# Optimization experiments

Measured on AMD Instinct MI355X. Metric: run time of the kernel, lower is better.

## Reference

```python
import jax, jax.numpy as jnp
import numpy as np

# --- module constants (from init_kwargs) ---
BETA = 0.95
UTE = 1.0001
DELAY = 7
CHOSEN_W1 = 0.5
THRESHOLD = 1.0      # snntorch Leaky default threshold
ALPHA = 2.0          # snntorch ATan surrogate default alpha
T, B = 4096, 4096
SPIKE_PROB = 0.02    # sparse binary spike trains


@jax.custom_vjp
def spike_fn(x):
    # Heaviside forward; ATan surrogate gradient in backward (snntorch default)
    return (x > 0).astype(x.dtype)

def _spike_fwd(x):
    return spike_fn(x), x

def _spike_bwd(x, g):
    return (g * (ALPHA / 2.0) / (1.0 + (jnp.pi / 2.0 * ALPHA * x) ** 2),)

spike_fn.defvjp(_spike_fwd, _spike_bwd)


def setup_inputs() -> dict:
    key = jax.random.key(0)
    k1, _ = jax.random.split(key)
    spike_seq = (jax.random.uniform(k1, (T, B, 2)) < SPIKE_PROB).astype(jnp.float32)
    # calculate_weights(delay): w1 = chosen_w1; w2 = ute - beta**delay * w1
    w1 = CHOSEN_W1
    w2 = UTE - BETA ** DELAY * w1
    W = jnp.array([[w1, w2]], dtype=jnp.float32)  # fc.weight, shape [1, 2]
    return {"spike_seq": spike_seq, "W": W}


def reference(spike_seq, W):
    # spike_seq: [T, B, 2], W: [1, 2] -> spk_rec: [T, B, 1]
    # Precompute all linear currents in one GEMM (same math as per-step fc)
    cur_seq = jnp.einsum('tbi,oi->tbo', spike_seq, W)  # [T, B, 1]

    def step(mem, cur):
        # snntorch Leaky (reset_mechanism='subtract'):
        #   reset computed from PREVIOUS mem (detached heaviside)
        reset = (mem > THRESHOLD).astype(mem.dtype)
        mem_new = BETA * mem + cur - reset * THRESHOLD
        spk = spike_fn(mem_new - THRESHOLD)
        return mem_new, spk

    mem0 = jnp.zeros((spike_seq.shape[1], 1), dtype=spike_seq.dtype)
    _, spk_rec = jax.lax.scan(step, mem0, cur_seq)
    return spk_rec
```

## Files before the change

kernel.cpp:

```cpp
#include <hip/hip_runtime.h>
#include <stdint.h>


#define T_STEPS 4096
#define B_NEUR  4096
#define NCHUNK  32
#define CH_W    8
#define WARM_W  48
#define KG      (T_STEPS / 16)

typedef float f4v __attribute__((ext_vector_type(4)));

__global__ __launch_bounds__(256) void fmfm_compress(
    const f4v*  __restrict__ sp4,
    uint32_t*   __restrict__ codes)
{
    const int tid = blockIdx.x * 256 + threadIdx.x;
    const int b2  = tid & (B_NEUR / 2 - 1);
    const int kg  = tid >> 11;
    const f4v* p = sp4 + (size_t)kg * 16 * (B_NEUR / 2) + b2;
    uint32_t we = 0, wo = 0;
    #pragma unroll
    for (int i = 0; i < 16; ++i) {
        f4v s = __builtin_nontemporal_load(p + (size_t)i * (B_NEUR / 2));
        uint32_t ce = (s.x != 0.0f ? 1u : 0u) | (s.y != 0.0f ? 2u : 0u);
        uint32_t co = (s.z != 0.0f ? 1u : 0u) | (s.w != 0.0f ? 2u : 0u);
        we |= ce << (2 * i);
        wo |= co << (2 * i);
    }
    *reinterpret_cast<uint2*>(codes + (size_t)kg * B_NEUR + 2 * b2) =
        make_uint2(we, wo);
}

__global__ __launch_bounds__(256) void fmfm_scanA(
    const uint32_t* __restrict__ codes,
    const float*    __restrict__ W,
    float*          __restrict__ out,
    uint4*          __restrict__ spec)
{
    __shared__ float2 lut2[16];

    const float w1  = W[0];
    const float w2  = W[1];
    const float w12 = __fadd_rn(w1, w2);

    if (threadIdx.x < 16) {
        uint32_t e = threadIdx.x;
        uint32_t c0 = e & 3u, c1 = (e >> 2) & 3u;
        float2 v;
        v.x = (c0 & 1u) ? ((c0 & 2u) ? w12 : w1) : ((c0 & 2u) ? w2 : 0.0f);
        v.y = (c1 & 1u) ? ((c1 & 2u) ? w12 : w1) : ((c1 & 2u) ? w2 : 0.0f);
        lut2[e] = v;
    }
    __syncthreads();

    const int tid = blockIdx.x * 256 + threadIdx.x;
    const int b   = tid & (B_NEUR - 1);
    const int c   = tid >> 12;
    const int body_w0 = c * CH_W;
    const int w_start = (body_w0 >= WARM_W) ? body_w0 - WARM_W : 0;
    const int w_end   = body_w0 + CH_W;
    const uint32_t* cp = codes + b;

#define CLD(IDX) cp[(size_t)((IDX) < w_end ? (IDX) : (w_end - 1)) * B_NEUR]
#define DECODE2(WORD, D)                                                  \
    {                                                                     \
        _Pragma("unroll")                                                 \
        for (int _j = 0; _j < 8; ++_j)                                    \
            D[_j] = lut2[((WORD) >> (4 * _j)) & 0xFu];                    \
    }
#define STEPN(CUR)                                                        \
    {                                                                     \
        float _m = __fsub_rn(__fadd_rn(__fmul_rn(0.95f, mem), (CUR)),     \
                             rst);                                        \
        rst = (_m > 1.0f) ? 1.0f : 0.0f;                                  \
        mem = _m;                                                         \
    }
#define STEPS_(CUR, Q, K)                                                 \
    {                                                                     \
        float _m = __fsub_rn(__fadd_rn(__fmul_rn(0.95f, mem), (CUR)),     \
                             rst);                                        \
        rst = (_m > 1.0f) ? 1.0f : 0.0f;                                  \
        mem = _m;                                                         \
        __builtin_nontemporal_store(rst, (Q) + (size_t)(K) * B_NEUR);     \
    }
#define CHAIN16N(D)                                                       \
    {                                                                     \
        _Pragma("unroll")                                                 \
        for (int _j = 0; _j < 8; ++_j) { STEPN(D[_j].x) STEPN(D[_j].y) }  \
    }
#define CHAIN16S(D, WIDX)                                                 \
    {                                                                     \
        float* _q = out + (size_t)(WIDX) * 16 * B_NEUR + b;               \
        _Pragma("unroll")                                                 \
        for (int _j = 0; _j < 8; ++_j) {                                  \
            STEPS_(D[_j].x, _q, 2 * _j)                                   \
            STEPS_(D[_j].y, _q, 2 * _j + 1)                               \
        }                                                                 \
    }

    uint32_t pa = CLD(w_start);
    uint32_t pb = CLD(w_start + 1);
    uint32_t pc = CLD(w_start + 2);
    uint32_t pd = CLD(w_start + 3);

    float2 dA[8], dB[8];
    DECODE2(pa, dA)

    float mem = 0.0f, rst = 0.0f;

    for (int iw = w_start; iw < body_w0; iw += 2) {
        uint32_t t0 = CLD(iw + 4);
        DECODE2(pb, dB)
        CHAIN16N(dA)
        pa = pb; pb = pc; pc = pd; pd = t0;
        uint32_t t1 = CLD(iw + 5);
        DECODE2(pb, dA)
        CHAIN16N(dB)
        pa = pb; pb = pc; pc = pd; pd = t1;
    }

    const float sm = mem;
    const float sr = rst;

    for (int iw = body_w0; iw < w_end; iw += 2) {
        uint32_t t0 = CLD(iw + 4);
        DECODE2(pb, dB)
        CHAIN16S(dA, iw)
        pa = pb; pb = pc; pc = pd; pd = t0;
        uint32_t t1 = CLD(iw + 5);
        DECODE2(pb, dA)
        CHAIN16S(dB, iw + 1)
        pa = pb; pb = pc; pc = pd; pd = t1;
    }

    uint4 sv;
    sv.x = __float_as_uint(sm);
    sv.y = (sr != 0.0f) ? 1u : 0u;
    sv.z = __float_as_uint(mem);
    sv.w = (rst != 0.0f) ? 1u : 0u;
    spec[(size_t)c * B_NEUR + b] = sv;

#undef CLD
#undef DECODE2
#undef STEPN
#undef STEPS_
#undef CHAIN16N
#undef CHAIN16S
}

__global__ __launch_bounds__(64) void fmfm_scanB(
    const uint32_t* __restrict__ codes,
    const float*    __restrict__ W,
    float*          __restrict__ out,
    const uint4*    __restrict__ spec)
{
    const int b = blockIdx.x * 64 + threadIdx.x;
    const float w1  = W[0];
    const float w2  = W[1];
    const float w12 = __fadd_rn(w1, w2);

    float mem = 0.0f, rst = 0.0f;
    uint4 sn = spec[b];
    for (int c = 0; c < NCHUNK; ++c) {
        uint4 s = sn;
        if (c + 1 < NCHUNK) sn = spec[(size_t)(c + 1) * B_NEUR + b];
        bool ok = (s.x == __float_as_uint(mem)) &&
                  ((s.y != 0u) == (rst != 0.0f));
        if (ok) {
            mem = __uint_as_float(s.z);
            rst = s.w ? 1.0f : 0.0f;
        } else {
            for (int wi = 0; wi < CH_W; ++wi) {
                uint32_t w = codes[(size_t)(c * CH_W + wi) * B_NEUR + b];
                float* q = out + (size_t)(c * CH_W + wi) * 16 * B_NEUR + b;
                #pragma unroll
                for (int j = 0; j < 16; ++j) {
                    uint32_t cc = (w >> (2 * j)) & 3u;
                    float cur = (cc & 1u) ? ((cc & 2u) ? w12 : w1)
                                          : ((cc & 2u) ? w2 : 0.0f);
                    float m = __fsub_rn(__fadd_rn(__fmul_rn(0.95f, mem), cur),
                                        rst);
                    rst = (m > 1.0f) ? 1.0f : 0.0f;
                    mem = m;
                    q[(size_t)j * B_NEUR] = rst;
                }
            }
        }
    }
}

__global__ __launch_bounds__(64) void fmfm_scan_fused(
    const float2* __restrict__ sp, const float* __restrict__ W,
    float* __restrict__ out)
{
    const int b = blockIdx.x * 64 + threadIdx.x;
    const float w1 = W[0];
    const float w2 = W[1];
    const float2* p = sp + b;
    float* q = out + b;
    float mem = 0.0f, rst = 0.0f;
    #pragma unroll 8
    for (int t = 0; t < T_STEPS; ++t) {
        float2 s = p[(size_t)t * B_NEUR];
        float cur = __fadd_rn(__fmul_rn(s.x, w1), __fmul_rn(s.y, w2));
        float m = __fsub_rn(__fadd_rn(__fmul_rn(0.95f, mem), cur), rst);
        float spk = (m > 1.0f) ? 1.0f : 0.0f;
        q[(size_t)t * B_NEUR] = spk;
        mem = m;
        rst = spk;
    }
}

extern "C" void kernel_launch(void* const* d_in, const int* in_sizes, int n_in,
                              void* d_out, int out_size, void* d_ws, size_t ws_size,
                              hipStream_t stream) {
    const f4v*   sp4 = (const f4v*)d_in[0];
    const float* W   = (const float*)d_in[1];
    float*       out = (float*)d_out;

    const size_t codes_bytes = (size_t)KG * B_NEUR * 4;
    const size_t spec_bytes  = (size_t)NCHUNK * B_NEUR * 16;
    if (ws_size < codes_bytes + spec_bytes) {
        fmfm_scan_fused<<<dim3(B_NEUR / 64), dim3(64), 0, stream>>>(
            (const float2*)d_in[0], W, out);
        return;
    }
    uint32_t* codes = (uint32_t*)d_ws;
    uint4*    spec  = (uint4*)((char*)d_ws + codes_bytes);

    fmfm_compress<<<dim3(KG * (B_NEUR / 2) / 256), dim3(256), 0, stream>>>(sp4, codes);
    fmfm_scanA<<<dim3(NCHUNK * B_NEUR / 256), dim3(256), 0, stream>>>(codes, W, out, spec);
    fmfm_scanB<<<dim3(B_NEUR / 64), dim3(64), 0, stream>>>(codes, W, out, spec);
}
```

Before: 60.21 us.

## Pack spike bits in LDS and write output as coalesced float4 stores

Result: faster. 58.04 us (-3.6%).

```diff
diff --git a/kernel.cpp b/kernel.cpp
--- a/kernel.cpp
+++ b/kernel.cpp
@@ -4,8 +4,8 @@
 
 #define T_STEPS 4096
 #define B_NEUR  4096
-#define NCHUNK  32
-#define CH_W    8
+#define NCHUNK  16
+#define CH_W    16
 #define WARM_W  48
 #define KG      (T_STEPS / 16)
 
@@ -38,7 +38,8 @@
     float*          __restrict__ out,
     uint4*          __restrict__ spec)
 {
-    __shared__ float2 lut2[16];
+    __shared__ float2   lut2[16];
+    __shared__ uint32_t lbits[256];
 
     const float w1  = W[0];
     const float w2  = W[1];
@@ -57,6 +58,7 @@
     const int tid = blockIdx.x * 256 + threadIdx.x;
     const int b   = tid & (B_NEUR - 1);
     const int c   = tid >> 12;
+    const int b0  = (blockIdx.x * 256) & (B_NEUR - 1);
     const int body_w0 = c * CH_W;
     const int w_start = (body_w0 >= WARM_W) ? body_w0 - WARM_W : 0;
     const int w_end   = body_w0 + CH_W;
@@ -76,26 +78,26 @@
         rst = (_m > 1.0f) ? 1.0f : 0.0f;                                  \
         mem = _m;                                                         \
     }
-#define STEPS_(CUR, Q, K)                                                 \
+#define STEPB(CUR, POS)                                                   \
     {                                                                     \
         float _m = __fsub_rn(__fadd_rn(__fmul_rn(0.95f, mem), (CUR)),     \
                              rst);                                        \
-        rst = (_m > 1.0f) ? 1.0f : 0.0f;                                  \
+        uint32_t _sb = (_m > 1.0f) ? 1u : 0u;                             \
+        bits |= _sb << (POS);                                             \
+        rst = _sb ? 1.0f : 0.0f;                                          \
         mem = _m;                                                         \
-        __builtin_nontemporal_store(rst, (Q) + (size_t)(K) * B_NEUR);     \
     }
 #define CHAIN16N(D)                                                       \
     {                                                                     \
         _Pragma("unroll")                                                 \
         for (int _j = 0; _j < 8; ++_j) { STEPN(D[_j].x) STEPN(D[_j].y) }  \
     }
-#define CHAIN16S(D, WIDX)                                                 \
-    {                                                                     \
-        float* _q = out + (size_t)(WIDX) * 16 * B_NEUR + b;               \
+#define CHAIN16B(D, HALF)                                                 \
+    {                                                                     \
         _Pragma("unroll")                                                 \
         for (int _j = 0; _j < 8; ++_j) {                                  \
-            STEPS_(D[_j].x, _q, 2 * _j)                                   \
-            STEPS_(D[_j].y, _q, 2 * _j + 1)                               \
+            STEPB(D[_j].x, ((HALF) << 4) + 2 * _j)                        \
+            STEPB(D[_j].y, ((HALF) << 4) + 2 * _j + 1)                    \
         }                                                                 \
     }
 
@@ -123,15 +125,34 @@
     const float sm = mem;
     const float sr = rst;
 
+    const int q  = threadIdx.x & 63;
+    const int th = threadIdx.x >> 6;
     for (int iw = body_w0; iw < w_end; iw += 2) {
+        uint32_t bits = 0;
         uint32_t t0 = CLD(iw + 4);
         DECODE2(pb, dB)
-        CHAIN16S(dA, iw)
+        CHAIN16B(dA, 0)
         pa = pb; pb = pc; pc = pd; pd = t0;
         uint32_t t1 = CLD(iw + 5);
         DECODE2(pb, dA)
-        CHAIN16S(dB, iw + 1)
+        CHAIN16B(dB, 1)
         pa = pb; pb = pc; pc = pd; pd = t1;
+
+        lbits[threadIdx.x] = bits;
+        __syncthreads();
+        const uint4 bw = *reinterpret_cast<const uint4*>(&lbits[4 * q]);
+        float* qp = out + (size_t)iw * 16 * B_NEUR + b0 + 4 * q;
+        #pragma unroll
+        for (int r = 0; r < 8; ++r) {
+            const int tp = th * 8 + r;
+            f4v v;
+            v.x = ((bw.x >> tp) & 1u) ? 1.0f : 0.0f;
+            v.y = ((bw.y >> tp) & 1u) ? 1.0f : 0.0f;
+            v.z = ((bw.z >> tp) & 1u) ? 1.0f : 0.0f;
+            v.w = ((bw.w >> tp) & 1u) ? 1.0f : 0.0f;
+            *reinterpret_cast<f4v*>(qp + (size_t)tp * B_NEUR) = v;
+        }
+        __syncthreads();
     }
 
     uint4 sv;
@@ -144,9 +165,9 @@
 #undef CLD
 #undef DECODE2
 #undef STEPN
-#undef STEPS_
+#undef STEPB
 #undef CHAIN16N
-#undef CHAIN16S
+#undef CHAIN16B
 }
 
 __global__ __launch_bounds__(64) void fmfm_scanB(
```
